# Performance work log

Hardware: AMD Instinct MI355X
Metric: run time of the kernel (lower is better)

Reference implementation:

```python
import jax, jax.numpy as jnp
import numpy as np

B, T, D = 2, 1024, 2048
E, K, H = 64, 4, 512          # n_experts, top-k, expert_dim
S, HS = 2, H * K              # shared experts, shared hidden dim
CAP = 512


def setup_inputs() -> dict:
    key = jax.random.key(0)
    ks = jax.random.split(key, 9)
    scale = 0.02
    return {
        "x": jax.random.normal(ks[0], (B, T, D), jnp.float32),
        "Wr": jax.random.normal(ks[1], (D, E), jnp.float32) * scale,
        "router_bias": jnp.zeros((E,), jnp.float32),
        "Wg": jax.random.normal(ks[2], (E, D, H), jnp.float32) * scale,
        "Wu": jax.random.normal(ks[3], (E, D, H), jnp.float32) * scale,
        "Wd": jax.random.normal(ks[4], (E, H, D), jnp.float32) * scale,
        "Sg": jax.random.normal(ks[5], (S, D, HS), jnp.float32) * scale,
        "Su": jax.random.normal(ks[6], (S, D, HS), jnp.float32) * scale,
        "Sd": jax.random.normal(ks[7], (S, HS, D), jnp.float32) * scale,
    }


def reference(x, Wr, router_bias, Wg, Wu, Wd, Sg, Su, Sd):
    Bx, Tx, Dx = x.shape
    N = Bx * Tx
    flat = x.reshape(N, Dx)                              # [N, D]

    # ---- router ----
    logits = flat @ Wr + router_bias                     # [N, E]
    scores = jax.nn.softmax(logits, axis=-1)
    topk_scores, topk_idx = jax.lax.top_k(scores, K)     # [N, K]
    topk_scores = topk_scores / topk_scores.sum(-1, keepdims=True)

    eid = topk_idx.reshape(-1)                           # [N*K] expert per assignment
    w = topk_scores.reshape(-1)                          # [N*K] combine weight
    tok = jnp.repeat(jnp.arange(N), K)                   # [N*K] source token id

    # position of each assignment within its expert's buffer
    oh = jax.nn.one_hot(eid, E, dtype=jnp.int32)         # [N*K, E]
    pos = ((jnp.cumsum(oh, axis=0) * oh).sum(-1) - 1)    # [N*K]
    valid = pos < CAP

    # ---- dispatch: scatter tokens into per-expert buffers ----
    xb = jnp.zeros((E, CAP, Dx), x.dtype).at[eid, pos].set(flat[tok], mode="drop")

    # ---- grouped SwiGLU expert FFN ----
    h = jax.nn.silu(jnp.einsum("ecd,edh->ech", xb, Wg)) * jnp.einsum("ecd,edh->ech", xb, Wu)
    yb = jnp.einsum("ech,ehd->ecd", h, Wd)               # [E, CAP, D]

    # ---- combine: gather back and weighted scatter-add to tokens ----
    y = yb[eid, jnp.minimum(pos, CAP - 1)] * (w * valid)[:, None]
    out = jnp.zeros((N, Dx), x.dtype).at[tok].add(y)

    # ---- always-on shared experts ----
    hs = jax.nn.silu(jnp.einsum("nd,sdh->nsh", flat, Sg)) * jnp.einsum("nd,sdh->nsh", flat, Su)
    out = out + jnp.einsum("nsh,shd->nd", hs, Sd)

    return out.reshape(Bx, Tx, Dx)
```

## Files before the change

### kernel.cpp

```cpp
#include <hip/hip_runtime.h>
#include <hip/hip_bf16.h>
#include <stdint.h>

#define N_TOK 2048
#define DM    2048
#define NEXP  64
#define TOPK  4
#define HEXP  512
#define CAPC  512
#define NSH   2
#define HSH   2048
#define RTB   8

typedef __attribute__((ext_vector_type(8))) short short8;
typedef __attribute__((ext_vector_type(4))) float f32x4;
typedef __attribute__((ext_vector_type(4))) float f4;
typedef __attribute__((ext_vector_type(4))) unsigned uint4v;

#define GLDS16(g, l) __builtin_amdgcn_global_load_lds(                     \
    (const __attribute__((address_space(1))) void*)(g),                    \
    (__attribute__((address_space(3))) void*)(l), 16, 0, 0)

#define VMWAIT(N) asm volatile("s_waitcnt vmcnt(" #N ")" ::: "memory")
#define BARX() do { asm volatile("" ::: "memory");                          \
                    __builtin_amdgcn_s_barrier();                           \
                    asm volatile("" ::: "memory"); } while (0)

static __device__ __forceinline__ unsigned short f2bf(float f) {
  union { float f; unsigned u; } v; v.f = f;
  unsigned r = v.u + 0x7FFFu + ((v.u >> 16) & 1u);
  return (unsigned short)(r >> 16);
}

__global__ __launch_bounds__(256) void k_convert(const float* __restrict__ x,
                                                 unsigned short* __restrict__ xb) {
  int i = (blockIdx.x * 256 + threadIdx.x) * 8;
  f4 a = *(const f4*)(x + i);
  f4 b = *(const f4*)(x + i + 4);
  short8 o;
  o[0]=f2bf(a[0]); o[1]=f2bf(a[1]); o[2]=f2bf(a[2]); o[3]=f2bf(a[3]);
  o[4]=f2bf(b[0]); o[5]=f2bf(b[1]); o[6]=f2bf(b[2]); o[7]=f2bf(b[3]);
  *(short8*)(xb + i) = o;
}

#define ARGMAX_ROUND(S,I)                                            \
  { float bv = v; int bi = lane;                                     \
    _Pragma("unroll")                                                \
    for (int o = 32; o; o >>= 1) {                                   \
      float ov = __shfl_xor(bv, o); int oi = __shfl_xor(bi, o);      \
      if (ov > bv || (ov == bv && oi < bi)) { bv = ov; bi = oi; }    \
    }                                                                \
    S = bv; I = bi; if (lane == bi) v = -1.f; }

__global__ __launch_bounds__(256) void k_router(const float* __restrict__ x,
    const float* __restrict__ Wr, const float* __restrict__ bias,
    int* __restrict__ cnt, int* __restrict__ lists, float* __restrict__ wlist) {
  __shared__ float part[4][RTB][64];
  __shared__ float logits[RTB][64];
  int t = threadIdx.x;
  int e = t & 63, sl = t >> 6;
  int tok0 = blockIdx.x * RTB;
  const float* xp = x + (size_t)tok0 * DM;
  float acc[RTB];
#pragma unroll
  for (int i = 0; i < RTB; ++i) acc[i] = 0.f;
  for (int d = sl * 512; d < sl * 512 + 512; ++d) {
    float w = Wr[(size_t)d * NEXP + e];
#pragma unroll
    for (int i = 0; i < RTB; ++i) acc[i] += xp[(size_t)i * DM + d] * w;
  }
#pragma unroll
  for (int i = 0; i < RTB; ++i) part[sl][i][e] = acc[i];
  __syncthreads();
  for (int i = sl; i < RTB; i += 4)
    logits[i][e] = part[0][i][e] + part[1][i][e] + part[2][i][e] + part[3][i][e] + bias[e];
  __syncthreads();
  int lane = t & 63, wv = t >> 6;
  for (int i = wv * 2; i < wv * 2 + 2; ++i) {
    float lg = logits[i][lane];
    float m = lg;
#pragma unroll
    for (int o = 32; o; o >>= 1) m = fmaxf(m, __shfl_xor(m, o));
    float p = expf(lg - m);
    float sm = p;
#pragma unroll
    for (int o = 32; o; o >>= 1) sm += __shfl_xor(sm, o);
    float v = p / sm;
    float s0, s1, s2, s3; int i0, i1, i2, i3;
    ARGMAX_ROUND(s0, i0)
    ARGMAX_ROUND(s1, i1)
    ARGMAX_ROUND(s2, i2)
    ARGMAX_ROUND(s3, i3)
    float tot = s0 + s1 + s2 + s3;
    if (lane < TOPK) {
      float myw = (lane == 0 ? s0 : lane == 1 ? s1 : lane == 2 ? s2 : s3) / tot;
      int   mye = (lane == 0 ? i0 : lane == 1 ? i1 : lane == 2 ? i2 : i3);
      int pos = atomicAdd(&cnt[mye], 1);
      if (pos < CAPC) {
        lists[mye * CAPC + pos] = tok0 + i;
        wlist[mye * CAPC + pos] = myw;
      }
    }
  }
}

__global__ void k_offs(const int* __restrict__ cnt, int* __restrict__ offs) {
  int l = threadIdx.x;
  int c = min(cnt[l], CAPC);
  int sum = c;
#pragma unroll
  for (int o = 1; o < 64; o <<= 1) {
    int ov = __shfl_up(sum, o);
    if (l >= o) sum += ov;
  }
  offs[l + 1] = sum;
  if (l == 0) offs[0] = 0;
}


static __device__ __forceinline__ short8 frag_ldA(const unsigned short* lds, int row, int kElem) {
  int byte = row * 64 + kElem * 2;
  byte ^= ((row >> 1) & 3) << 4;
  return *(const short8*)((const char*)lds + byte);
}

static __device__ __forceinline__ short8 bfragB(const float* lB, int nl, int kb) {
  const float* p = lB + kb * 64 + (nl ^ (((kb >> 3) & 1) << 4));
  float f0 = p[0],   f1 = p[64],  f2 = p[128], f3 = p[192];
  float f4_ = p[256], f5 = p[320], f6 = p[384], f7 = p[448];
  unsigned u0, u1, u2, u3;
  asm("v_cvt_pk_bf16_f32 %0, %1, %2" : "=v"(u0) : "v"(f0),  "v"(f1));
  asm("v_cvt_pk_bf16_f32 %0, %1, %2" : "=v"(u1) : "v"(f2),  "v"(f3));
  asm("v_cvt_pk_bf16_f32 %0, %1, %2" : "=v"(u2) : "v"(f4_), "v"(f5));
  asm("v_cvt_pk_bf16_f32 %0, %1, %2" : "=v"(u3) : "v"(f6),  "v"(f7));
  uint4v uv = {u0, u1, u2, u3};
  return __builtin_bit_cast(short8, uv);
}

static __device__ __forceinline__ void mma1f(const unsigned short* lA, const float* lB,
    f32x4 (&acc)[4][2], int wm, int wn, int lane) {
  int r16 = lane & 15;
  int kb  = (lane >> 4) * 8;
  short8 a[4], b[2];
#pragma unroll
  for (int mf = 0; mf < 4; ++mf) a[mf] = frag_ldA(lA, wm + mf * 16 + r16, kb);
#pragma unroll
  for (int nf = 0; nf < 2; ++nf) b[nf] = bfragB(lB, wn + nf * 16 + r16, kb);
#pragma unroll
  for (int mf = 0; mf < 4; ++mf)
#pragma unroll
    for (int nf = 0; nf < 2; ++nf)
      acc[mf][nf] = __builtin_amdgcn_mfma_f32_16x16x32_bf16(a[mf], b[nf], acc[mf][nf], 0, 0, 0);
}

static __device__ __forceinline__ void mma2f(const unsigned short* lA,
    const float* lBg, const float* lBu,
    f32x4 (&accg)[4][2], f32x4 (&accu)[4][2], int wm, int wn, int lane) {
  int r16 = lane & 15;
  int kb  = (lane >> 4) * 8;
  short8 a[4], bg[2], bu[2];
#pragma unroll
  for (int mf = 0; mf < 4; ++mf) a[mf] = frag_ldA(lA, wm + mf * 16 + r16, kb);
#pragma unroll
  for (int nf = 0; nf < 2; ++nf) {
    bg[nf] = bfragB(lBg, wn + nf * 16 + r16, kb);
    bu[nf] = bfragB(lBu, wn + nf * 16 + r16, kb);
  }
#pragma unroll
  for (int mf = 0; mf < 4; ++mf)
#pragma unroll
    for (int nf = 0; nf < 2; ++nf) {
      accg[mf][nf] = __builtin_amdgcn_mfma_f32_16x16x32_bf16(a[mf], bg[nf], accg[mf][nf], 0, 0, 0);
      accu[mf][nf] = __builtin_amdgcn_mfma_f32_16x16x32_bf16(a[mf], bu[nf], accu[mf][nf], 0, 0, 0);
    }
}

static __device__ __forceinline__ float silu_mul(float g, float u) {
  return g / (1.f + expf(-g)) * u;
}

#define A_SETUP(asrc, SROW_EXPR)                                            \
  const unsigned short* asrc[2];                                            \
  {                                                                         \
    _Pragma("unroll")                                                       \
    for (int p = 0; p < 2; ++p) {                                           \
      int row = p * 64 + wv * 16 + (lane >> 2);                             \
      int srow = (SROW_EXPR);                                               \
      asrc[p] = Abase + (size_t)srow * lda                                  \
              + (((lane & 3) ^ ((row >> 1) & 3)) << 3);                     \
    }                                                                       \
  }
#define A_STAGE(asrc, lAbuf, k0)                                            \
  { _Pragma("unroll")                                                       \
    for (int p = 0; p < 2; ++p)                                             \
      GLDS16(asrc[p] + (k0), (lAbuf) + p * 2048 + wv * 512); }

#define B_SETUP(bsrc, Bbase, ldb)                                           \
  const float* bsrc[2];                                                     \
  {                                                                         \
    _Pragma("unroll")                                                       \
    for (int p = 0; p < 2; ++p) {                                           \
      int k = p * 16 + wv * 4 + (lane >> 4);                                \
      int c = (lane & 15) ^ (((k >> 3) & 1) << 2);                          \
      bsrc[p] = (Bbase) + (size_t)k * (ldb) + n0 + c * 4;                   \
    }                                                                       \
  }
#define B_STAGE(bsrc, lBbuf, k0, ldb)                                       \
  { _Pragma("unroll")                                                       \
    for (int p = 0; p < 2; ++p)                                             \
      GLDS16(bsrc[p] + (size_t)(k0) * (ldb), (lBbuf) + p * 1024 + wv * 256); }

__global__ __launch_bounds__(256, 3) void k_expert_gateup(const unsigned short* __restrict__ xbf,
    const float* __restrict__ Wg, const float* __restrict__ Wu,
    const int* __restrict__ cnt, const int* __restrict__ offs,
    const int* __restrict__ lists, unsigned short* __restrict__ hws) {
  int e = blockIdx.y;
  int ne = min(cnt[e], CAPC);
  if (ne == 0) return;
  int n0 = blockIdx.x * 64;
  const float* Bg = Wg + (size_t)e * DM * HEXP;
  const float* Bu = Wu + (size_t)e * DM * HEXP;
  const int* lst = lists + e * CAPC;
  int base = offs[e];
  __shared__ unsigned short lA[2][128 * 32];
  __shared__ float lBg[2][32 * 64];
  __shared__ float lBu[2][32 * 64];
  int tid = threadIdx.x;
  int lane = tid & 63, wv = tid >> 6;
  int wm = (wv >> 1) * 64, wn = (wv & 1) * 32;
  const unsigned short* Abase = xbf; const int lda = DM;
  B_SETUP(bgsrc, Bg, HEXP)
  B_SETUP(busrc, Bu, HEXP)
  const int NT = DM / 32;
  for (int m0 = 0; m0 < ne; m0 += 128) {
    A_SETUP(asrc, lst[min(m0 + row, ne - 1)])
    f32x4 accg[4][2] = {};
    f32x4 accu[4][2] = {};
    A_STAGE(asrc, lA[0], 0)  B_STAGE(bgsrc, lBg[0], 0, HEXP)  B_STAGE(busrc, lBu[0], 0, HEXP)
    A_STAGE(asrc, lA[1], 32) B_STAGE(bgsrc, lBg[1], 32, HEXP) B_STAGE(busrc, lBu[1], 32, HEXP)
    VMWAIT(6); BARX();
#pragma unroll 1
    for (int t = 0; t < NT; t += 2) {
      mma2f(lA[0], lBg[0], lBu[0], accg, accu, wm, wn, lane);
      BARX();
      if (t + 2 < NT) {
        int k2 = (t + 2) * 32;
        A_STAGE(asrc, lA[0], k2) B_STAGE(bgsrc, lBg[0], k2, HEXP) B_STAGE(busrc, lBu[0], k2, HEXP)
        VMWAIT(6);
      } else { VMWAIT(0); }
      BARX();
      mma2f(lA[1], lBg[1], lBu[1], accg, accu, wm, wn, lane);
      if (t + 2 < NT) {
        BARX();
        if (t + 3 < NT) {
          int k3 = (t + 3) * 32;
          A_STAGE(asrc, lA[1], k3) B_STAGE(bgsrc, lBg[1], k3, HEXP) B_STAGE(busrc, lBu[1], k3, HEXP)
          VMWAIT(6);
        } else { VMWAIT(0); }
        BARX();
      }
    }
    BARX();
#pragma unroll
    for (int mf = 0; mf < 4; ++mf)
#pragma unroll
      for (int r = 0; r < 4; ++r) {
        int rl = m0 + wm + mf * 16 + (lane >> 4) * 4 + r;
        if (rl < ne) {
#pragma unroll
          for (int nf = 0; nf < 2; ++nf) {
            int col = n0 + wn + nf * 16 + (lane & 15);
            float h = silu_mul(accg[mf][nf][r], accu[mf][nf][r]);
            hws[(size_t)(base + rl) * HEXP + col] = f2bf(h);
          }
        }
      }
  }
}

__global__ __launch_bounds__(256, 3) void k_shared_gateup(const unsigned short* __restrict__ xbf,
    const float* __restrict__ Sg, const float* __restrict__ Su,
    unsigned short* __restrict__ hs) {
  int n0 = blockIdx.x * 64;
  int m0 = blockIdx.y * 128;
  int s  = blockIdx.z;
  const float* Bg = Sg + (size_t)s * DM * HSH;
  const float* Bu = Su + (size_t)s * DM * HSH;
  __shared__ unsigned short lA[2][128 * 32];
  __shared__ float lBg[2][32 * 64];
  __shared__ float lBu[2][32 * 64];
  int tid = threadIdx.x;
  int lane = tid & 63, wv = tid >> 6;
  int wm = (wv >> 1) * 64, wn = (wv & 1) * 32;
  const unsigned short* Abase = xbf; const int lda = DM;
  B_SETUP(bgsrc, Bg, HSH)
  B_SETUP(busrc, Bu, HSH)
  A_SETUP(asrc, m0 + row)
  f32x4 accg[4][2] = {};
  f32x4 accu[4][2] = {};
  const int NT = DM / 32;
  A_STAGE(asrc, lA[0], 0)  B_STAGE(bgsrc, lBg[0], 0, HSH)  B_STAGE(busrc, lBu[0], 0, HSH)
  A_STAGE(asrc, lA[1], 32) B_STAGE(bgsrc, lBg[1], 32, HSH) B_STAGE(busrc, lBu[1], 32, HSH)
  VMWAIT(6); BARX();
#pragma unroll 1
  for (int t = 0; t < NT; t += 2) {
    mma2f(lA[0], lBg[0], lBu[0], accg, accu, wm, wn, lane);
    BARX();
    if (t + 2 < NT) {
      int k2 = (t + 2) * 32;
      A_STAGE(asrc, lA[0], k2) B_STAGE(bgsrc, lBg[0], k2, HSH) B_STAGE(busrc, lBu[0], k2, HSH)
      VMWAIT(6);
    } else { VMWAIT(0); }
    BARX();
    mma2f(lA[1], lBg[1], lBu[1], accg, accu, wm, wn, lane);
    if (t + 2 < NT) {
      BARX();
      if (t + 3 < NT) {
        int k3 = (t + 3) * 32;
        A_STAGE(asrc, lA[1], k3) B_STAGE(bgsrc, lBg[1], k3, HSH) B_STAGE(busrc, lBu[1], k3, HSH)
        VMWAIT(6);
      } else { VMWAIT(0); }
      BARX();
    }
  }
#pragma unroll
  for (int mf = 0; mf < 4; ++mf)
#pragma unroll
    for (int nf = 0; nf < 2; ++nf)
#pragma unroll
      for (int r = 0; r < 4; ++r) {
        int row = m0 + wm + mf * 16 + (lane >> 4) * 4 + r;
        int col = n0 + wn + nf * 16 + (lane & 15);
        float h = silu_mul(accg[mf][nf][r], accu[mf][nf][r]);
        hs[(size_t)row * (NSH * HSH) + s * HSH + col] = f2bf(h);
      }
}

__global__ __launch_bounds__(256, 4) void k_shared_down(const unsigned short* __restrict__ hs,
    const float* __restrict__ Sd, float* __restrict__ out) {
  int n0 = blockIdx.x * 64;
  int m0 = blockIdx.y * 128;
  __shared__ unsigned short lA[2][128 * 32];
  __shared__ float lB[2][32 * 64];
  int tid = threadIdx.x;
  int lane = tid & 63, wv = tid >> 6;
  int wm = (wv >> 1) * 64, wn = (wv & 1) * 32;
  const unsigned short* Abase = hs; const int lda = NSH * HSH;
  B_SETUP(bsrc, Sd, DM)
  A_SETUP(asrc, m0 + row)
  f32x4 acc[4][2] = {};
  const int NT = (NSH * HSH) / 32;
  A_STAGE(asrc, lA[0], 0)  B_STAGE(bsrc, lB[0], 0, DM)
  A_STAGE(asrc, lA[1], 32) B_STAGE(bsrc, lB[1], 32, DM)
  VMWAIT(4); BARX();
#pragma unroll 1
  for (int t = 0; t < NT; t += 2) {
    mma1f(lA[0], lB[0], acc, wm, wn, lane);
    BARX();
    if (t + 2 < NT) {
      int k2 = (t + 2) * 32;
      A_STAGE(asrc, lA[0], k2) B_STAGE(bsrc, lB[0], k2, DM)
      VMWAIT(4);
    } else { VMWAIT(0); }
    BARX();
    mma1f(lA[1], lB[1], acc, wm, wn, lane);
    if (t + 2 < NT) {
      BARX();
      if (t + 3 < NT) {
        int k3 = (t + 3) * 32;
        A_STAGE(asrc, lA[1], k3) B_STAGE(bsrc, lB[1], k3, DM)
        VMWAIT(4);
      } else { VMWAIT(0); }
      BARX();
    }
  }
#pragma unroll
  for (int mf = 0; mf < 4; ++mf)
#pragma unroll
    for (int nf = 0; nf < 2; ++nf)
#pragma unroll
      for (int r = 0; r < 4; ++r) {
        int row = m0 + wm + mf * 16 + (lane >> 4) * 4 + r;
        int col = n0 + wn + nf * 16 + (lane & 15);
        out[(size_t)row * DM + col] = acc[mf][nf][r];
      }
}

__global__ __launch_bounds__(256, 4) void k_expert_down(const unsigned short* __restrict__ hws,
    const float* __restrict__ Wd, const int* __restrict__ cnt, const int* __restrict__ offs,
    const int* __restrict__ lists, const float* __restrict__ wlist,
    float* __restrict__ out) {
  int e = blockIdx.y;
  int ne = min(cnt[e], CAPC);
  if (ne == 0) return;
  int n0 = blockIdx.x * 64;
  const float* B = Wd + (size_t)e * HEXP * DM;
  __shared__ unsigned short lA[2][128 * 32];
  __shared__ float lB[2][32 * 64];
  int tid = threadIdx.x;
  int lane = tid & 63, wv = tid >> 6;
  int wm = (wv >> 1) * 64, wn = (wv & 1) * 32;
  const unsigned short* Abase = hws + (size_t)offs[e] * HEXP; const int lda = HEXP;
  B_SETUP(bsrc, B, DM)
  const int NT = HEXP / 32;
  for (int m0 = 0; m0 < ne; m0 += 128) {
    A_SETUP(asrc, min(m0 + row, ne - 1))
    f32x4 acc[4][2] = {};
    A_STAGE(asrc, lA[0], 0)  B_STAGE(bsrc, lB[0], 0, DM)
    A_STAGE(asrc, lA[1], 32) B_STAGE(bsrc, lB[1], 32, DM)
    VMWAIT(4); BARX();
#pragma unroll 1
    for (int t = 0; t < NT; t += 2) {
      mma1f(lA[0], lB[0], acc, wm, wn, lane);
      BARX();
      if (t + 2 < NT) {
        int k2 = (t + 2) * 32;
        A_STAGE(asrc, lA[0], k2) B_STAGE(bsrc, lB[0], k2, DM)
        VMWAIT(4);
      } else { VMWAIT(0); }
      BARX();
      mma1f(lA[1], lB[1], acc, wm, wn, lane);
      if (t + 2 < NT) {
        BARX();
        if (t + 3 < NT) {
          int k3 = (t + 3) * 32;
          A_STAGE(asrc, lA[1], k3) B_STAGE(bsrc, lB[1], k3, DM)
          VMWAIT(4);
        } else { VMWAIT(0); }
        BARX();
      }
    }
    BARX();
#pragma unroll
    for (int mf = 0; mf < 4; ++mf)
#pragma unroll
      for (int r = 0; r < 4; ++r) {
        int rl = m0 + wm + mf * 16 + (lane >> 4) * 4 + r;
        if (rl < ne) {
          int tok  = lists[e * CAPC + rl];
          float w  = wlist[e * CAPC + rl];
#pragma unroll
          for (int nf = 0; nf < 2; ++nf) {
            int col = n0 + wn + nf * 16 + (lane & 15);
            atomicAdd(out + (size_t)tok * DM + col, acc[mf][nf][r] * w);
          }
        }
      }
  }
}

extern "C" void kernel_launch(void* const* d_in, const int* in_sizes, int n_in,
                              void* d_out, int out_size, void* d_ws, size_t ws_size,
                              hipStream_t stream) {
  const float* x    = (const float*)d_in[0];
  const float* Wr   = (const float*)d_in[1];
  const float* bias = (const float*)d_in[2];
  const float* Wg   = (const float*)d_in[3];
  const float* Wu   = (const float*)d_in[4];
  const float* Wd   = (const float*)d_in[5];
  const float* Sg   = (const float*)d_in[6];
  const float* Su   = (const float*)d_in[7];
  const float* Sd   = (const float*)d_in[8];
  float* out = (float*)d_out;
  char* ws = (char*)d_ws;

  const size_t off_cnt   = 0;
  const size_t off_offs  = 256;
  const size_t off_lists = 1024;
  const size_t off_wlist = off_lists + (size_t)NEXP * CAPC * 4;
  const size_t off_xbf   = off_wlist + (size_t)NEXP * CAPC * 4;
  const size_t off_hs    = off_xbf + (size_t)N_TOK * DM * 2;
  const size_t off_h     = off_hs + (size_t)N_TOK * NSH * HSH * 2;
  const size_t req       = off_h + (size_t)N_TOK * TOPK * HEXP * 2;
  if (ws_size < req) return;

  int* cnt            = (int*)(ws + off_cnt);
  int* offs           = (int*)(ws + off_offs);
  int* lists          = (int*)(ws + off_lists);
  float* wlist        = (float*)(ws + off_wlist);
  unsigned short* xbf = (unsigned short*)(ws + off_xbf);
  unsigned short* hs  = (unsigned short*)(ws + off_hs);
  unsigned short* hws = (unsigned short*)(ws + off_h);

  hipMemsetAsync(cnt, 0, NEXP * sizeof(int), stream);
  k_convert<<<(N_TOK * DM) / (256 * 8), 256, 0, stream>>>(x, xbf);
  k_router<<<N_TOK / RTB, 256, 0, stream>>>(x, Wr, bias, cnt, lists, wlist);
  k_offs<<<1, 64, 0, stream>>>(cnt, offs);
  k_expert_gateup<<<dim3(HEXP / 64, NEXP), 256, 0, stream>>>(xbf, Wg, Wu, cnt, offs, lists, hws);
  k_shared_gateup<<<dim3(HSH / 64, N_TOK / 128, NSH), 256, 0, stream>>>(xbf, Sg, Su, hs);
  k_shared_down<<<dim3(DM / 64, N_TOK / 128), 256, 0, stream>>>(hs, Sd, out);
  k_expert_down<<<dim3(DM / 64, NEXP), 256, 0, stream>>>(hws, Wd, cnt, offs, lists, wlist, out);
}
```

Measured before the change: 662.5 us.

## Retile GEMMs to 256x32 blocks with XCD-aware workgroup swizzle

Changes every GEMM kernel from a 128x64 tile with 2x2 waves to a 256x32 tile where each wave owns 64 full rows, so each B (fp32 weight) tile is narrower and each expert's token rows fit in one or two M passes. The grids are flattened to 1D and remapped with an XCD swizzle so that consecutive blocks sharing an expert or row panel land on the same XCD and can reuse its L2. This halves redundant weight loads per token chunk but doubles A reloads across N and raises LDS for A, which may reduce occupancy.

```diff
diff --git a/kernel.cpp b/kernel.cpp
--- a/kernel.cpp
+++ b/kernel.cpp
@@ -30,6 +30,10 @@
   union { float f; unsigned u; } v; v.f = f;
   unsigned r = v.u + 0x7FFFu + ((v.u >> 16) & 1u);
   return (unsigned short)(r >> 16);
+}
+
+static __device__ __forceinline__ int swz_xcd(int id, int nwg) {
+  return (id & 7) * (nwg >> 3) + (id >> 3);
 }
 
 __global__ __launch_bounds__(256) void k_convert(const float* __restrict__ x,
@@ -125,9 +129,9 @@
 }
 
 static __device__ __forceinline__ short8 bfragB(const float* lB, int nl, int kb) {
-  const float* p = lB + kb * 64 + (nl ^ (((kb >> 3) & 1) << 4));
-  float f0 = p[0],   f1 = p[64],  f2 = p[128], f3 = p[192];
-  float f4_ = p[256], f5 = p[320], f6 = p[384], f7 = p[448];
+  const float* p = lB + kb * 32 + (nl ^ (((kb >> 3) & 1) << 4));
+  float f0 = p[0],   f1 = p[32],  f2 = p[64],  f3 = p[96];
+  float f4_ = p[128], f5 = p[160], f6 = p[192], f7 = p[224];
   unsigned u0, u1, u2, u3;
   asm("v_cvt_pk_bf16_f32 %0, %1, %2" : "=v"(u0) : "v"(f0),  "v"(f1));
   asm("v_cvt_pk_bf16_f32 %0, %1, %2" : "=v"(u1) : "v"(f2),  "v"(f3));
@@ -138,14 +142,14 @@
 }
 
 static __device__ __forceinline__ void mma1f(const unsigned short* lA, const float* lB,
-    f32x4 (&acc)[4][2], int wm, int wn, int lane) {
+    f32x4 (&acc)[4][2], int wm, int lane) {
   int r16 = lane & 15;
   int kb  = (lane >> 4) * 8;
   short8 a[4], b[2];
 #pragma unroll
   for (int mf = 0; mf < 4; ++mf) a[mf] = frag_ldA(lA, wm + mf * 16 + r16, kb);
 #pragma unroll
-  for (int nf = 0; nf < 2; ++nf) b[nf] = bfragB(lB, wn + nf * 16 + r16, kb);
+  for (int nf = 0; nf < 2; ++nf) b[nf] = bfragB(lB, nf * 16 + r16, kb);
 #pragma unroll
   for (int mf = 0; mf < 4; ++mf)
 #pragma unroll
@@ -155,7 +159,7 @@
 
 static __device__ __forceinline__ void mma2f(const unsigned short* lA,
     const float* lBg, const float* lBu,
-    f32x4 (&accg)[4][2], f32x4 (&accu)[4][2], int wm, int wn, int lane) {
+    f32x4 (&accg)[4][2], f32x4 (&accu)[4][2], int wm, int lane) {
   int r16 = lane & 15;
   int kb  = (lane >> 4) * 8;
   short8 a[4], bg[2], bu[2];
@@ -163,8 +167,8 @@
   for (int mf = 0; mf < 4; ++mf) a[mf] = frag_ldA(lA, wm + mf * 16 + r16, kb);
 #pragma unroll
   for (int nf = 0; nf < 2; ++nf) {
-    bg[nf] = bfragB(lBg, wn + nf * 16 + r16, kb);
-    bu[nf] = bfragB(lBu, wn + nf * 16 + r16, kb);
+    bg[nf] = bfragB(lBg, nf * 16 + r16, kb);
+    bu[nf] = bfragB(lBu, nf * 16 + r16, kb);
   }
 #pragma unroll
   for (int mf = 0; mf < 4; ++mf)
@@ -180,81 +184,73 @@
 }
 
 #define A_SETUP(asrc, SROW_EXPR)                                            \
-  const unsigned short* asrc[2];                                            \
-  {                                                                         \
-    _Pragma("unroll")                                                       \
-    for (int p = 0; p < 2; ++p) {                                           \
-      int row = p * 64 + wv * 16 + (lane >> 2);                             \
+  const unsigned short* asrc[4];                                            \
+  { _Pragma("unroll")                                                       \
+    for (int p = 0; p < 4; ++p) {                                           \
+      int row = wv * 64 + p * 16 + (lane >> 2);                             \
       int srow = (SROW_EXPR);                                               \
       asrc[p] = Abase + (size_t)srow * lda                                  \
               + (((lane & 3) ^ ((row >> 1) & 3)) << 3);                     \
-    }                                                                       \
-  }
+    } }
 #define A_STAGE(asrc, lAbuf, k0)                                            \
   { _Pragma("unroll")                                                       \
-    for (int p = 0; p < 2; ++p)                                             \
-      GLDS16(asrc[p] + (k0), (lAbuf) + p * 2048 + wv * 512); }
+    for (int p = 0; p < 4; ++p)                                             \
+      GLDS16(asrc[p] + (k0), (lAbuf) + wv * 2048 + p * 512); }
 
 #define B_SETUP(bsrc, Bbase, ldb)                                           \
-  const float* bsrc[2];                                                     \
-  {                                                                         \
-    _Pragma("unroll")                                                       \
-    for (int p = 0; p < 2; ++p) {                                           \
-      int k = p * 16 + wv * 4 + (lane >> 4);                                \
-      int c = (lane & 15) ^ (((k >> 3) & 1) << 2);                          \
-      bsrc[p] = (Bbase) + (size_t)k * (ldb) + n0 + c * 4;                   \
-    }                                                                       \
-  }
+  const float* bsrc;                                                        \
+  { int k = wv * 8 + (lane >> 3);                                           \
+    int c = (lane & 7) ^ (((k >> 3) & 1) << 2);                             \
+    bsrc = (Bbase) + (size_t)k * (ldb) + n0 + c * 4; }
 #define B_STAGE(bsrc, lBbuf, k0, ldb)                                       \
-  { _Pragma("unroll")                                                       \
-    for (int p = 0; p < 2; ++p)                                             \
-      GLDS16(bsrc[p] + (size_t)(k0) * (ldb), (lBbuf) + p * 1024 + wv * 256); }
+  GLDS16((bsrc) + (size_t)(k0) * (ldb), (lBbuf) + wv * 256)
 
 __global__ __launch_bounds__(256, 3) void k_expert_gateup(const unsigned short* __restrict__ xbf,
     const float* __restrict__ Wg, const float* __restrict__ Wu,
     const int* __restrict__ cnt, const int* __restrict__ offs,
     const int* __restrict__ lists, unsigned short* __restrict__ hws) {
-  int e = blockIdx.y;
+  int bid = swz_xcd(blockIdx.x, NEXP * (HEXP / 32));
+  int e  = bid >> 4;
+  int n0 = (bid & 15) * 32;
   int ne = min(cnt[e], CAPC);
   if (ne == 0) return;
-  int n0 = blockIdx.x * 64;
   const float* Bg = Wg + (size_t)e * DM * HEXP;
   const float* Bu = Wu + (size_t)e * DM * HEXP;
   const int* lst = lists + e * CAPC;
   int base = offs[e];
-  __shared__ unsigned short lA[2][128 * 32];
-  __shared__ float lBg[2][32 * 64];
-  __shared__ float lBu[2][32 * 64];
+  __shared__ unsigned short lA[2][256 * 32];
+  __shared__ float lBg[2][32 * 32];
+  __shared__ float lBu[2][32 * 32];
   int tid = threadIdx.x;
   int lane = tid & 63, wv = tid >> 6;
-  int wm = (wv >> 1) * 64, wn = (wv & 1) * 32;
+  int wm = wv * 64;
   const unsigned short* Abase = xbf; const int lda = DM;
   B_SETUP(bgsrc, Bg, HEXP)
   B_SETUP(busrc, Bu, HEXP)
   const int NT = DM / 32;
-  for (int m0 = 0; m0 < ne; m0 += 128) {
+  for (int m0 = 0; m0 < ne; m0 += 256) {
     A_SETUP(asrc, lst[min(m0 + row, ne - 1)])
     f32x4 accg[4][2] = {};
     f32x4 accu[4][2] = {};
-    A_STAGE(asrc, lA[0], 0)  B_STAGE(bgsrc, lBg[0], 0, HEXP)  B_STAGE(busrc, lBu[0], 0, HEXP)
-    A_STAGE(asrc, lA[1], 32) B_STAGE(bgsrc, lBg[1], 32, HEXP) B_STAGE(busrc, lBu[1], 32, HEXP)
+    A_STAGE(asrc, lA[0], 0)  B_STAGE(bgsrc, lBg[0], 0, HEXP);  B_STAGE(busrc, lBu[0], 0, HEXP);
+    A_STAGE(asrc, lA[1], 32) B_STAGE(bgsrc, lBg[1], 32, HEXP); B_STAGE(busrc, lBu[1], 32, HEXP);
     VMWAIT(6); BARX();
 #pragma unroll 1
     for (int t = 0; t < NT; t += 2) {
-      mma2f(lA[0], lBg[0], lBu[0], accg, accu, wm, wn, lane);
+      mma2f(lA[0], lBg[0], lBu[0], accg, accu, wm, lane);
       BARX();
       if (t + 2 < NT) {
         int k2 = (t + 2) * 32;
-        A_STAGE(asrc, lA[0], k2) B_STAGE(bgsrc, lBg[0], k2, HEXP) B_STAGE(busrc, lBu[0], k2, HEXP)
+        A_STAGE(asrc, lA[0], k2) B_STAGE(bgsrc, lBg[0], k2, HEXP); B_STAGE(busrc, lBu[0], k2, HEXP);
         VMWAIT(6);
       } else { VMWAIT(0); }
       BARX();
-      mma2f(lA[1], lBg[1], lBu[1], accg, accu, wm, wn, lane);
+      mma2f(lA[1], lBg[1], lBu[1], accg, accu, wm, lane);
       if (t + 2 < NT) {
         BARX();
         if (t + 3 < NT) {
           int k3 = (t + 3) * 32;
-          A_STAGE(asrc, lA[1], k3) B_STAGE(bgsrc, lBg[1], k3, HEXP) B_STAGE(busrc, lBu[1], k3, HEXP)
+          A_STAGE(asrc, lA[1], k3) B_STAGE(bgsrc, lBg[1], k3, HEXP); B_STAGE(busrc, lBu[1], k3, HEXP);
           VMWAIT(6);
         } else { VMWAIT(0); }
         BARX();
@@ -269,7 +265,7 @@
         if (rl < ne) {
 #pragma unroll
           for (int nf = 0; nf < 2; ++nf) {
-            int col = n0 + wn + nf * 16 + (lane & 15);
+            int col = n0 + nf * 16 + (lane & 15);
             float h = silu_mul(accg[mf][nf][r], accu[mf][nf][r]);
             hws[(size_t)(base + rl) * HEXP + col] = f2bf(h);
           }
@@ -281,17 +277,17 @@
 __global__ __launch_bounds__(256, 3) void k_shared_gateup(const unsigned short* __restrict__ xbf,
     const float* __restrict__ Sg, const float* __restrict__ Su,
     unsigned short* __restrict__ hs) {
-  int n0 = blockIdx.x * 64;
-  int m0 = blockIdx.y * 128;
-  int s  = blockIdx.z;
+  int bid = swz_xcd(blockIdx.x, NSH * (N_TOK / 256) * (HSH / 32));
+  int nb = bid & 63, mb = (bid >> 6) & 7, s = bid >> 9;
+  int n0 = nb * 32, m0 = mb * 256;
   const float* Bg = Sg + (size_t)s * DM * HSH;
   const float* Bu = Su + (size_t)s * DM * HSH;
-  __shared__ unsigned short lA[2][128 * 32];
-  __shared__ float lBg[2][32 * 64];
-  __shared__ float lBu[2][32 * 64];
+  __shared__ unsigned short lA[2][256 * 32];
+  __shared__ float lBg[2][32 * 32];
+  __shared__ float lBu[2][32 * 32];
   int tid = threadIdx.x;
   int lane = tid & 63, wv = tid >> 6;
-  int wm = (wv >> 1) * 64, wn = (wv & 1) * 32;
+  int wm = wv * 64;
   const unsigned short* Abase = xbf; const int lda = DM;
   B_SETUP(bgsrc, Bg, HSH)
   B_SETUP(busrc, Bu, HSH)
@@ -299,25 +295,25 @@
   f32x4 accg[4][2] = {};
   f32x4 accu[4][2] = {};
   const int NT = DM / 32;
-  A_STAGE(asrc, lA[0], 0)  B_STAGE(bgsrc, lBg[0], 0, HSH)  B_STAGE(busrc, lBu[0], 0, HSH)
-  A_STAGE(asrc, lA[1], 32) B_STAGE(bgsrc, lBg[1], 32, HSH) B_STAGE(busrc, lBu[1], 32, HSH)
+  A_STAGE(asrc, lA[0], 0)  B_STAGE(bgsrc, lBg[0], 0, HSH);  B_STAGE(busrc, lBu[0], 0, HSH);
+  A_STAGE(asrc, lA[1], 32) B_STAGE(bgsrc, lBg[1], 32, HSH); B_STAGE(busrc, lBu[1], 32, HSH);
   VMWAIT(6); BARX();
 #pragma unroll 1
   for (int t = 0; t < NT; t += 2) {
-    mma2f(lA[0], lBg[0], lBu[0], accg, accu, wm, wn, lane);
+    mma2f(lA[0], lBg[0], lBu[0], accg, accu, wm, lane);
     BARX();
     if (t + 2 < NT) {
       int k2 = (t + 2) * 32;
-      A_STAGE(asrc, lA[0], k2) B_STAGE(bgsrc, lBg[0], k2, HSH) B_STAGE(busrc, lBu[0], k2, HSH)
+      A_STAGE(asrc, lA[0], k2) B_STAGE(bgsrc, lBg[0], k2, HSH); B_STAGE(busrc, lBu[0], k2, HSH);
       VMWAIT(6);
     } else { VMWAIT(0); }
     BARX();
-    mma2f(lA[1], lBg[1], lBu[1], accg, accu, wm, wn, lane);
+    mma2f(lA[1], lBg[1], lBu[1], accg, accu, wm, lane);
     if (t + 2 < NT) {
       BARX();
       if (t + 3 < NT) {
         int k3 = (t + 3) * 32;
-        A_STAGE(asrc, lA[1], k3) B_STAGE(bgsrc, lBg[1], k3, HSH) B_STAGE(busrc, lBu[1], k3, HSH)
+        A_STAGE(asrc, lA[1], k3) B_STAGE(bgsrc, lBg[1], k3, HSH); B_STAGE(busrc, lBu[1], k3, HSH);
         VMWAIT(6);
       } else { VMWAIT(0); }
       BARX();
@@ -330,7 +326,7 @@
 #pragma unroll
       for (int r = 0; r < 4; ++r) {
         int row = m0 + wm + mf * 16 + (lane >> 4) * 4 + r;
-        int col = n0 + wn + nf * 16 + (lane & 15);
+        int col = n0 + nf * 16 + (lane & 15);
         float h = silu_mul(accg[mf][nf][r], accu[mf][nf][r]);
         hs[(size_t)row * (NSH * HSH) + s * HSH + col] = f2bf(h);
       }
@@ -338,38 +334,39 @@
 
 __global__ __launch_bounds__(256, 4) void k_shared_down(const unsigned short* __restrict__ hs,
     const float* __restrict__ Sd, float* __restrict__ out) {
-  int n0 = blockIdx.x * 64;
-  int m0 = blockIdx.y * 128;
-  __shared__ unsigned short lA[2][128 * 32];
-  __shared__ float lB[2][32 * 64];
+  int bid = swz_xcd(blockIdx.x, (N_TOK / 256) * (DM / 32));
+  int nb = bid & 63, mb = bid >> 6;
+  int n0 = nb * 32, m0 = mb * 256;
+  __shared__ unsigned short lA[2][256 * 32];
+  __shared__ float lB[2][32 * 32];
   int tid = threadIdx.x;
   int lane = tid & 63, wv = tid >> 6;
-  int wm = (wv >> 1) * 64, wn = (wv & 1) * 32;
+  int wm = wv * 64;
   const unsigned short* Abase = hs; const int lda = NSH * HSH;
   B_SETUP(bsrc, Sd, DM)
   A_SETUP(asrc, m0 + row)
   f32x4 acc[4][2] = {};
   const int NT = (NSH * HSH) / 32;
-  A_STAGE(asrc, lA[0], 0)  B_STAGE(bsrc, lB[0], 0, DM)
-  A_STAGE(asrc, lA[1], 32) B_STAGE(bsrc, lB[1], 32, DM)
-  VMWAIT(4); BARX();
+  A_STAGE(asrc, lA[0], 0)  B_STAGE(bsrc, lB[0], 0, DM);
+  A_STAGE(asrc, lA[1], 32) B_STAGE(bsrc, lB[1], 32, DM);
+  VMWAIT(5); BARX();
 #pragma unroll 1
   for (int t = 0; t < NT; t += 2) {
-    mma1f(lA[0], lB[0], acc, wm, wn, lane);
+    mma1f(lA[0], lB[0], acc, wm, lane);
     BARX();
     if (t + 2 < NT) {
       int k2 = (t + 2) * 32;
-      A_STAGE(asrc, lA[0], k2) B_STAGE(bsrc, lB[0], k2, DM)
-      VMWAIT(4);
+      A_STAGE(asrc, lA[0], k2) B_STAGE(bsrc, lB[0], k2, DM);
+      VMWAIT(5);
     } else { VMWAIT(0); }
     BARX();
-    mma1f(lA[1], lB[1], acc, wm, wn, lane);
+    mma1f(lA[1], lB[1], acc, wm, lane);
     if (t + 2 < NT) {
       BARX();
       if (t + 3 < NT) {
         int k3 = (t + 3) * 32;
-        A_STAGE(asrc, lA[1], k3) B_STAGE(bsrc, lB[1], k3, DM)
-        VMWAIT(4);
+        A_STAGE(asrc, lA[1], k3) B_STAGE(bsrc, lB[1], k3, DM);
+        VMWAIT(5);
       } else { VMWAIT(0); }
       BARX();
     }
@@ -381,7 +378,7 @@
 #pragma unroll
       for (int r = 0; r < 4; ++r) {
         int row = m0 + wm + mf * 16 + (lane >> 4) * 4 + r;
-        int col = n0 + wn + nf * 16 + (lane & 15);
+        int col = n0 + nf * 16 + (lane & 15);
         out[(size_t)row * DM + col] = acc[mf][nf][r];
       }
 }
@@ -390,42 +387,43 @@
     const float* __restrict__ Wd, const int* __restrict__ cnt, const int* __restrict__ offs,
     const int* __restrict__ lists, const float* __restrict__ wlist,
     float* __restrict__ out) {
-  int e = blockIdx.y;
+  int bid = swz_xcd(blockIdx.x, NEXP * (DM / 32));
+  int e  = bid >> 6;
+  int n0 = (bid & 63) * 32;
   int ne = min(cnt[e], CAPC);
   if (ne == 0) return;
-  int n0 = blockIdx.x * 64;
   const float* B = Wd + (size_t)e * HEXP * DM;
-  __shared__ unsigned short lA[2][128 * 32];
-  __shared__ float lB[2][32 * 64];
+  __shared__ unsigned short lA[2][256 * 32];
+  __shared__ float lB[2][32 * 32];
   int tid = threadIdx.x;
   int lane = tid & 63, wv = tid >> 6;
-  int wm = (wv >> 1) * 64, wn = (wv & 1) * 32;
+  int wm = wv * 64;
   const unsigned short* Abase = hws + (size_t)offs[e] * HEXP; const int lda = HEXP;
   B_SETUP(bsrc, B, DM)
   const int NT = HEXP / 32;
-  for (int m0 = 0; m0 < ne; m0 += 128) {
+  for (int m0 = 0; m0 < ne; m0 += 256) {
     A_SETUP(asrc, min(m0 + row, ne - 1))
     f32x4 acc[4][2] = {};
-    A_STAGE(asrc, lA[0], 0)  B_STAGE(bsrc, lB[0], 0, DM)
-    A_STAGE(asrc, lA[1], 32) B_STAGE(bsrc, lB[1], 32, DM)
-    VMWAIT(4); BARX();
+    A_STAGE(asrc, lA[0], 0)  B_STAGE(bsrc, lB[0], 0, DM);
+    A_STAGE(asrc, lA[1], 32) B_STAGE(bsrc, lB[1], 32, DM);
+    VMWAIT(5); BARX();
 #pragma unroll 1
     for (int t = 0; t < NT; t += 2) {
-      mma1f(lA[0], lB[0], acc, wm, wn, lane);
+      mma1f(lA[0], lB[0], acc, wm, lane);
       BARX();
       if (t + 2 < NT) {
         int k2 = (t + 2) * 32;
-        A_STAGE(asrc, lA[0], k2) B_STAGE(bsrc, lB[0], k2, DM)
-        VMWAIT(4);
+        A_STAGE(asrc, lA[0], k2) B_STAGE(bsrc, lB[0], k2, DM);
+        VMWAIT(5);
       } else { VMWAIT(0); }
       BARX();
-      mma1f(lA[1], lB[1], acc, wm, wn, lane);
+      mma1f(lA[1], lB[1], acc, wm, lane);
       if (t + 2 < NT) {
         BARX();
         if (t + 3 < NT) {
           int k3 = (t + 3) * 32;
-          A_STAGE(asrc, lA[1], k3) B_STAGE(bsrc, lB[1], k3, DM)
-          VMWAIT(4);
+          A_STAGE(asrc, lA[1], k3) B_STAGE(bsrc, lB[1], k3, DM);
+          VMWAIT(5);
         } else { VMWAIT(0); }
         BARX();
       }
@@ -441,7 +439,7 @@
           float w  = wlist[e * CAPC + rl];
 #pragma unroll
           for (int nf = 0; nf < 2; ++nf) {
-            int col = n0 + wn + nf * 16 + (lane & 15);
+            int col = n0 + nf * 16 + (lane & 15);
             atomicAdd(out + (size_t)tok * DM + col, acc[mf][nf][r] * w);
           }
         }
@@ -486,8 +484,8 @@
   k_convert<<<(N_TOK * DM) / (256 * 8), 256, 0, stream>>>(x, xbf);
   k_router<<<N_TOK / RTB, 256, 0, stream>>>(x, Wr, bias, cnt, lists, wlist);
   k_offs<<<1, 64, 0, stream>>>(cnt, offs);
-  k_expert_gateup<<<dim3(HEXP / 64, NEXP), 256, 0, stream>>>(xbf, Wg, Wu, cnt, offs, lists, hws);
-  k_shared_gateup<<<dim3(HSH / 64, N_TOK / 128, NSH), 256, 0, stream>>>(xbf, Sg, Su, hs);
-  k_shared_down<<<dim3(DM / 64, N_TOK / 128), 256, 0, stream>>>(hs, Sd, out);
-  k_expert_down<<<dim3(DM / 64, NEXP), 256, 0, stream>>>(hws, Wd, cnt, offs, lists, wlist, out);
-}
+  k_expert_gateup<<<NEXP * (HEXP / 32), 256, 0, stream>>>(xbf, Wg, Wu, cnt, offs, lists, hws);
+  k_shared_gateup<<<NSH * (N_TOK / 256) * (HSH / 32), 256, 0, stream>>>(xbf, Sg, Su, hs);
+  k_shared_down<<<(N_TOK / 256) * (DM / 32), 256, 0, stream>>>(hs, Sd, out);
+  k_expert_down<<<NEXP * (DM / 32), 256, 0, stream>>>(hws, Wd, cnt, offs, lists, wlist, out);
+}
```

Result: slower. 731.2 us (+10.4%).

## Split-K expert gate/up GEMM with bf16 LDS weights and atomic fp32 accumulation

Applied to the files above, without the earlier changes.

Replaces the fused expert gate/up kernel with a split-K version. Each block handles one matrix (gate or up), a quarter of K and half of N, and accumulates fp32 partial sums into global buffers with atomicAdd. A separate SwiGLU kernel then converts those sums to bf16. Weights are loaded into registers, converted to bf16 and written to swizzled LDS, which reduces LDS footprint and raises parallelism per expert. The cost is an extra memset of large fp32 accumulators, atomic traffic, and an additional elementwise pass.

```diff
diff --git a/kernel.cpp b/kernel.cpp
--- a/kernel.cpp
+++ b/kernel.cpp
@@ -22,9 +22,11 @@
     (__attribute__((address_space(3))) void*)(l), 16, 0, 0)
 
 #define VMWAIT(N) asm volatile("s_waitcnt vmcnt(" #N ")" ::: "memory")
+#define LGKM0()   asm volatile("s_waitcnt lgkmcnt(0)" ::: "memory")
 #define BARX() do { asm volatile("" ::: "memory");                          \
                     __builtin_amdgcn_s_barrier();                           \
                     asm volatile("" ::: "memory"); } while (0)
+#define MEMCLOB() asm volatile("" ::: "memory")
 
 static __device__ __forceinline__ unsigned short f2bf(float f) {
   union { float f; unsigned u; } v; v.f = f;
@@ -117,7 +119,6 @@
   if (l == 0) offs[0] = 0;
 }
 
-
 static __device__ __forceinline__ short8 frag_ldA(const unsigned short* lds, int row, int kElem) {
   int byte = row * 64 + kElem * 2;
   byte ^= ((row >> 1) & 3) << 4;
@@ -210,72 +211,158 @@
     for (int p = 0; p < 2; ++p)                                             \
       GLDS16(bsrc[p] + (size_t)(k0) * (ldb), (lBbuf) + p * 1024 + wv * 256); }
 
-__global__ __launch_bounds__(256, 3) void k_expert_gateup(const unsigned short* __restrict__ xbf,
+__global__ __launch_bounds__(512, 2) void k_expert_gu_mm(const unsigned short* __restrict__ xbf,
     const float* __restrict__ Wg, const float* __restrict__ Wu,
     const int* __restrict__ cnt, const int* __restrict__ offs,
-    const int* __restrict__ lists, unsigned short* __restrict__ hws) {
-  int e = blockIdx.y;
+    const int* __restrict__ lists, float* __restrict__ accg, float* __restrict__ accu) {
+  int bid = blockIdx.x;
+  int r8 = bid & 7, ns = (bid >> 3) & 1, q = bid >> 4;
+  int pair = q * 8 + r8;
+  int e = pair >> 3, mat = (pair >> 2) & 1, ks = pair & 3;
   int ne = min(cnt[e], CAPC);
   if (ne == 0) return;
-  int n0 = blockIdx.x * 64;
-  const float* Bg = Wg + (size_t)e * DM * HEXP;
-  const float* Bu = Wu + (size_t)e * DM * HEXP;
   const int* lst = lists + e * CAPC;
   int base = offs[e];
+  const float* W = (mat ? Wu : Wg) + (size_t)e * DM * HEXP;
+  float* accb = mat ? accu : accg;
+  int kr = ks * 512;
+  int nr = ns * 256;
+
   __shared__ unsigned short lA[2][128 * 32];
-  __shared__ float lBg[2][32 * 64];
-  __shared__ float lBu[2][32 * 64];
+  __shared__ unsigned short lB[2][32 * 256];
+
   int tid = threadIdx.x;
   int lane = tid & 63, wv = tid >> 6;
-  int wm = (wv >> 1) * 64, wn = (wv & 1) * 32;
-  const unsigned short* Abase = xbf; const int lda = DM;
-  B_SETUP(bgsrc, Bg, HEXP)
-  B_SETUP(busrc, Bu, HEXP)
-  const int NT = DM / 32;
+  int wm = (wv >> 2) * 64, wn = (wv & 3) * 64;
+  int r16 = lane & 15;
+  int kb  = (lane >> 4) * 8;
+
+  int kB = tid >> 4;
+  int nB = (tid & 15) * 16;
+  int swzB = (kB & 7) ^ ((kB >> 3) << 1);
+  const float* Wrow = W + (size_t)(kr + kB) * HEXP + nr + nB;
+  int wb_off  = kB * 512 + ((((nB >> 3) ^ swzB) & 31) << 4);
+  int wb_off2 = kB * 512 + (((((nB >> 3) + 1) ^ swzB) & 31) << 4);
+
+  const int NT = 16;
+
+#define AGU_BLOAD(dst, t)                                                   \
+  { const f4* p_ = (const f4*)(Wrow + (size_t)(t) * 32 * HEXP);             \
+    dst[0] = p_[0]; dst[1] = p_[1]; dst[2] = p_[2]; dst[3] = p_[3]; }
+
+#define AGU_BWRITE(buf, src)                                                \
+  { unsigned u0_, u1_, u2_, u3_;                                            \
+    asm("v_cvt_pk_bf16_f32 %0, %1, %2" : "=v"(u0_) : "v"(src[0][0]), "v"(src[0][1])); \
+    asm("v_cvt_pk_bf16_f32 %0, %1, %2" : "=v"(u1_) : "v"(src[0][2]), "v"(src[0][3])); \
+    asm("v_cvt_pk_bf16_f32 %0, %1, %2" : "=v"(u2_) : "v"(src[1][0]), "v"(src[1][1])); \
+    asm("v_cvt_pk_bf16_f32 %0, %1, %2" : "=v"(u3_) : "v"(src[1][2]), "v"(src[1][3])); \
+    uint4v v0_ = {u0_, u1_, u2_, u3_};                                      \
+    asm("v_cvt_pk_bf16_f32 %0, %1, %2" : "=v"(u0_) : "v"(src[2][0]), "v"(src[2][1])); \
+    asm("v_cvt_pk_bf16_f32 %0, %1, %2" : "=v"(u1_) : "v"(src[2][2]), "v"(src[2][3])); \
+    asm("v_cvt_pk_bf16_f32 %0, %1, %2" : "=v"(u2_) : "v"(src[3][0]), "v"(src[3][1])); \
+    asm("v_cvt_pk_bf16_f32 %0, %1, %2" : "=v"(u3_) : "v"(src[3][2]), "v"(src[3][3])); \
+    uint4v v1_ = {u0_, u1_, u2_, u3_};                                      \
+    *(short8*)((char*)(buf) + wb_off)  = __builtin_bit_cast(short8, v0_);   \
+    *(short8*)((char*)(buf) + wb_off2) = __builtin_bit_cast(short8, v1_); }
+
+#define AGU_AISSUE(buf, t) GLDS16(aptr + (size_t)(t) * 32, (unsigned short*)(buf) + wv * 512)
+
+#define AGU_MMA(la, lb)                                                     \
+  { short8 afr_[4];                                                         \
+    _Pragma("unroll")                                                       \
+    for (int mf = 0; mf < 4; ++mf) afr_[mf] = frag_ldA((la), wm + mf * 16 + r16, kb); \
+    _Pragma("unroll")                                                       \
+    for (int nf = 0; nf < 4; ++nf) {                                        \
+      int n_ = wn + nf * 16 + r16;                                          \
+      short8 bfr_;                                                          \
+      _Pragma("unroll")                                                     \
+      for (int j = 0; j < 8; ++j) {                                         \
+        int k_ = kb + j;                                                    \
+        int ch_ = (((n_ >> 3) ^ (k_ & 7) ^ ((k_ >> 3) << 1)) & 31);         \
+        bfr_[j] = *(const short*)((const char*)(lb) + k_ * 512 + (ch_ << 4) + (n_ & 7) * 2); \
+      }                                                                     \
+      _Pragma("unroll")                                                     \
+      for (int mf = 0; mf < 4; ++mf)                                        \
+        acc[mf][nf] = __builtin_amdgcn_mfma_f32_16x16x32_bf16(afr_[mf], bfr_, acc[mf][nf], 0, 0, 0); \
+    } }
+
   for (int m0 = 0; m0 < ne; m0 += 128) {
-    A_SETUP(asrc, lst[min(m0 + row, ne - 1)])
-    f32x4 accg[4][2] = {};
-    f32x4 accu[4][2] = {};
-    A_STAGE(asrc, lA[0], 0)  B_STAGE(bgsrc, lBg[0], 0, HEXP)  B_STAGE(busrc, lBu[0], 0, HEXP)
-    A_STAGE(asrc, lA[1], 32) B_STAGE(bgsrc, lBg[1], 32, HEXP) B_STAGE(busrc, lBu[1], 32, HEXP)
-    VMWAIT(6); BARX();
+    int arow = wv * 16 + (lane >> 2);
+    int srow = lst[min(m0 + arow, ne - 1)];
+    const unsigned short* aptr = xbf + (size_t)srow * DM + kr
+                               + (((lane & 3) ^ ((arow >> 1) & 3)) << 3);
+    f32x4 acc[4][4] = {};
+    f4 br0[4], br1[4];
+    AGU_BLOAD(br0, 0) MEMCLOB();
+    AGU_AISSUE(lA[0], 0); MEMCLOB();
+    AGU_BLOAD(br1, 1) MEMCLOB();
+    AGU_AISSUE(lA[1], 1); MEMCLOB();
+    VMWAIT(6);
+    AGU_BWRITE(lB[0], br0)
+    VMWAIT(5);
+    LGKM0(); BARX();
 #pragma unroll 1
     for (int t = 0; t < NT; t += 2) {
-      mma2f(lA[0], lBg[0], lBu[0], accg, accu, wm, wn, lane);
-      BARX();
-      if (t + 2 < NT) {
-        int k2 = (t + 2) * 32;
-        A_STAGE(asrc, lA[0], k2) B_STAGE(bgsrc, lBg[0], k2, HEXP) B_STAGE(busrc, lBu[0], k2, HEXP)
-        VMWAIT(6);
-      } else { VMWAIT(0); }
-      BARX();
-      mma2f(lA[1], lBg[1], lBu[1], accg, accu, wm, wn, lane);
-      if (t + 2 < NT) {
-        BARX();
+      AGU_MMA(lA[0], lB[0])
+      {
+        VMWAIT(1);
+        AGU_BWRITE(lB[1], br1)
+        VMWAIT(0);
+        LGKM0(); BARX();
+        if (t + 2 < NT) {
+          AGU_BLOAD(br0, t + 2) MEMCLOB();
+          AGU_AISSUE(lA[0], t + 2); MEMCLOB();
+        }
+      }
+      AGU_MMA(lA[1], lB[1])
+      if (t + 1 < NT - 1) {
+        VMWAIT(1);
+        AGU_BWRITE(lB[0], br0)
+        VMWAIT(0);
+        LGKM0(); BARX();
         if (t + 3 < NT) {
-          int k3 = (t + 3) * 32;
-          A_STAGE(asrc, lA[1], k3) B_STAGE(bgsrc, lBg[1], k3, HEXP) B_STAGE(busrc, lBu[1], k3, HEXP)
-          VMWAIT(6);
-        } else { VMWAIT(0); }
-        BARX();
+          AGU_BLOAD(br1, t + 3) MEMCLOB();
+          AGU_AISSUE(lA[1], t + 3); MEMCLOB();
+        }
       }
     }
-    BARX();
 #pragma unroll
     for (int mf = 0; mf < 4; ++mf)
 #pragma unroll
-      for (int r = 0; r < 4; ++r) {
-        int rl = m0 + wm + mf * 16 + (lane >> 4) * 4 + r;
-        if (rl < ne) {
-#pragma unroll
-          for (int nf = 0; nf < 2; ++nf) {
-            int col = n0 + wn + nf * 16 + (lane & 15);
-            float h = silu_mul(accg[mf][nf][r], accu[mf][nf][r]);
-            hws[(size_t)(base + rl) * HEXP + col] = f2bf(h);
+      for (int nf = 0; nf < 4; ++nf)
+#pragma unroll
+        for (int rr = 0; rr < 4; ++rr) {
+          int rl = m0 + wm + mf * 16 + (lane >> 4) * 4 + rr;
+          if (rl < ne) {
+            int col = nr + wn + nf * 16 + r16;
+            atomicAdd(accb + (size_t)(base + rl) * HEXP + col, acc[mf][nf][rr]);
           }
         }
-      }
-  }
+    BARX();
+  }
+#undef AGU_BLOAD
+#undef AGU_BWRITE
+#undef AGU_AISSUE
+#undef AGU_MMA
+}
+
+__global__ __launch_bounds__(256) void k_swiglu(const float* __restrict__ accg,
+    const float* __restrict__ accu, const int* __restrict__ offs,
+    unsigned short* __restrict__ hws) {
+  int total = offs[NEXP];
+  int gid = blockIdx.x * 256 + threadIdx.x;
+  int row = gid >> 6;
+  if (row >= total) return;
+  int c0 = (gid & 63) * 8;
+  size_t o = (size_t)row * HEXP + c0;
+  f4 g0 = *(const f4*)(accg + o), g1 = *(const f4*)(accg + o + 4);
+  f4 u0 = *(const f4*)(accu + o), u1 = *(const f4*)(accu + o + 4);
+  short8 out;
+  out[0] = f2bf(silu_mul(g0[0], u0[0])); out[1] = f2bf(silu_mul(g0[1], u0[1]));
+  out[2] = f2bf(silu_mul(g0[2], u0[2])); out[3] = f2bf(silu_mul(g0[3], u0[3]));
+  out[4] = f2bf(silu_mul(g1[0], u1[0])); out[5] = f2bf(silu_mul(g1[1], u1[1]));
+  out[6] = f2bf(silu_mul(g1[2], u1[2])); out[7] = f2bf(silu_mul(g1[3], u1[3]));
+  *(short8*)(hws + o) = out;
 }
 
 __global__ __launch_bounds__(256, 3) void k_shared_gateup(const unsigned short* __restrict__ xbf,
@@ -471,7 +558,9 @@
   const size_t off_xbf   = off_wlist + (size_t)NEXP * CAPC * 4;
   const size_t off_hs    = off_xbf + (size_t)N_TOK * DM * 2;
   const size_t off_h     = off_hs + (size_t)N_TOK * NSH * HSH * 2;
-  const size_t req       = off_h + (size_t)N_TOK * TOPK * HEXP * 2;
+  const size_t off_accg  = (off_h + (size_t)N_TOK * TOPK * HEXP * 2 + 255) & ~(size_t)255;
+  const size_t off_accu  = off_accg + (size_t)N_TOK * TOPK * HEXP * 4;
+  const size_t req       = off_accu + (size_t)N_TOK * TOPK * HEXP * 4;
   if (ws_size < req) return;
 
   int* cnt            = (int*)(ws + off_cnt);
@@ -481,12 +570,16 @@
   unsigned short* xbf = (unsigned short*)(ws + off_xbf);
   unsigned short* hs  = (unsigned short*)(ws + off_hs);
   unsigned short* hws = (unsigned short*)(ws + off_h);
+  float* accg         = (float*)(ws + off_accg);
+  float* accu         = (float*)(ws + off_accu);
 
   hipMemsetAsync(cnt, 0, NEXP * sizeof(int), stream);
+  hipMemsetAsync(accg, 0, (size_t)N_TOK * TOPK * HEXP * 8, stream);
   k_convert<<<(N_TOK * DM) / (256 * 8), 256, 0, stream>>>(x, xbf);
   k_router<<<N_TOK / RTB, 256, 0, stream>>>(x, Wr, bias, cnt, lists, wlist);
   k_offs<<<1, 64, 0, stream>>>(cnt, offs);
-  k_expert_gateup<<<dim3(HEXP / 64, NEXP), 256, 0, stream>>>(xbf, Wg, Wu, cnt, offs, lists, hws);
+  k_expert_gu_mm<<<NEXP * 2 * 4 * 2, 512, 0, stream>>>(xbf, Wg, Wu, cnt, offs, lists, accg, accu);
+  k_swiglu<<<(N_TOK * TOPK * HEXP / 8) / 256, 256, 0, stream>>>(accg, accu, offs, hws);
   k_shared_gateup<<<dim3(HSH / 64, N_TOK / 128, NSH), 256, 0, stream>>>(xbf, Sg, Su, hs);
   k_shared_down<<<dim3(DM / 64, N_TOK / 128), 256, 0, stream>>>(hs, Sd, out);
   k_expert_down<<<dim3(DM / 64, NEXP), 256, 0, stream>>>(hws, Wd, cnt, offs, lists, wlist, out);
```

Measured after the change: 727.6 us. +9.8%, slower.
